# Optimization experiments

Measured on AMD Instinct MI355X. Metric: run time of the kernel, lower is better.

Reference implementation:

```python
import jax, jax.numpy as jnp
import numpy as np

UNITS = 1024
PRENET = 256
NMELS = 80
OPS = 2
ZONEOUT = 0.1  # deterministic (inference) zoneout blend


def _mi_lstm(x, wx, wh, alpha, b1, b2, bias):
    """Multiplicative-integration LSTM with deterministic zoneout.
    x: [B,T,D]; wx: [D,4U]; wh: [U,4U]; alpha/b1/b2/bias: [4U]."""
    B = x.shape[0]
    U = wh.shape[0]
    xw = jnp.einsum('btd,dk->btk', x, wx)  # precompute input projection [B,T,4U]

    def step(carry, xw_t):
        h, c = carry
        hw = h @ wh  # [B,4U]
        z = alpha * xw_t * hw + b1 * xw_t + b2 * hw + bias
        i, f, g, o = jnp.split(z, 4, axis=-1)
        c_new = jax.nn.sigmoid(f) * c + jax.nn.sigmoid(i) * jnp.tanh(g)
        h_new = jax.nn.sigmoid(o) * jnp.tanh(c_new)
        c_out = ZONEOUT * c + (1.0 - ZONEOUT) * c_new
        h_out = ZONEOUT * h + (1.0 - ZONEOUT) * h_new
        return (h_out, c_out), h_out

    init = (jnp.zeros((B, U), x.dtype), jnp.zeros((B, U), x.dtype))
    _, hs = jax.lax.scan(step, init, jnp.swapaxes(xw, 0, 1))  # [T,B,U]
    return jnp.swapaxes(hs, 0, 1)


def setup_inputs() -> dict:
    key = jax.random.key(0)
    ks = jax.random.split(key, 10)
    s = 0.02
    w = lambda k, shape: (jax.random.normal(k, shape, jnp.float32) * s)
    G = 4 * UNITS
    return {
        'x': jax.random.normal(ks[0], (32, 400, NMELS), jnp.float32),
        'pw1': w(ks[1], (NMELS, PRENET)), 'pb1': jnp.zeros((PRENET,), jnp.float32),
        'pw2': w(ks[2], (PRENET, PRENET)), 'pb2': jnp.zeros((PRENET,), jnp.float32),
        'wx1': w(ks[3], (PRENET, G)), 'wh1': w(ks[4], (UNITS, G)),
        'a1': jnp.ones((G,), jnp.float32), 'b11': jnp.full((G,), 0.5, jnp.float32),
        'b21': jnp.full((G,), 0.5, jnp.float32), 'bias1': jnp.zeros((G,), jnp.float32),
        'wx2': w(ks[5], (UNITS, G)), 'wh2': w(ks[6], (UNITS, G)),
        'a2': jnp.ones((G,), jnp.float32), 'b12': jnp.full((G,), 0.5, jnp.float32),
        'b22': jnp.full((G,), 0.5, jnp.float32), 'bias2': jnp.zeros((G,), jnp.float32),
        'sw': w(ks[7], (UNITS, 1)), 'sb': jnp.zeros((1,), jnp.float32),
        'fw': w(ks[8], (UNITS, NMELS * OPS)), 'fb': jnp.zeros((NMELS * OPS,), jnp.float32),
    }


def reference(x, pw1, pb1, pw2, pb2, wx1, wh1, a1, b11, b21, bias1,
              wx2, wh2, a2, b12, b22, bias2, sw, sb, fw, fb):
    # prenet (dropout inactive in inference-mode reference)
    p = jax.nn.relu(x @ pw1 + pb1)
    p = jax.nn.relu(p @ pw2 + pb2)
    h1 = _mi_lstm(p, wx1, wh1, a1, b11, b21, bias1)
    h2 = _mi_lstm(h1, wx2, wh2, a2, b12, b22, bias2)
    stop = jax.nn.sigmoid(h2 @ sw + sb)          # [B,T,1]
    frames = h2 @ fw + fb                         # [B,T,160] linear projection
    return jnp.concatenate([frames, stop], axis=-1)  # [B,T,161]
```

## Files before the change

### kernel.cpp

```cpp
#include <hip/hip_runtime.h>
#include <hip/hip_fp16.h>
#include <math.h>

#define B_   32
#define T_   400
#define BT_  12800
#define U_   1024
#define G4_  4096
#define TCH  100
#define NCH  4

typedef _Float16 f16x8 __attribute__((ext_vector_type(8)));
typedef float    f32x4 __attribute__((ext_vector_type(4)));

__device__ __forceinline__ float sigf(float x){ return 1.0f/(1.0f+expf(-x)); }
__device__ __forceinline__ int f2h2(float a, float b){
    __half2 h = __floats2half2_rn(a, b);
    return __builtin_bit_cast(int, h);
}
__device__ __forceinline__ f16x8 ldg8(const __half* p){
    return *reinterpret_cast<const f16x8*>(p);
}

__global__ __launch_bounds__(256) void ws_sentinel_kernel(float* __restrict__ out, int n)
{
    const int i = blockIdx.x * 256 + threadIdx.x;
    if (i < n) out[i] = 1000.0f;
}

__global__ __launch_bounds__(256) void transpose_fp16_kernel(
    const float* __restrict__ W, __half* __restrict__ WT, int rowsTotal)
{
    __shared__ float tile[64][65];
    const int bx = blockIdx.x;
    const int by = blockIdx.y;
    const int tid = threadIdx.x;
    for (int i = tid; i < 1024; i += 256) {
        const int r  = i >> 4;
        const int c4 = (i & 15) * 4;
        float4 v = *(const float4*)&W[(by*64 + r)*G4_ + bx*64 + c4];
        tile[c4+0][r] = v.x; tile[c4+1][r] = v.y;
        tile[c4+2][r] = v.z; tile[c4+3][r] = v.w;
    }
    __syncthreads();
    for (int i = tid; i < 512; i += 256) {
        const int c  = i >> 3;
        const int r8 = (i & 7) * 8;
        int4 pk;
        pk.x = f2h2(tile[c][r8+0], tile[c][r8+1]);
        pk.y = f2h2(tile[c][r8+2], tile[c][r8+3]);
        pk.z = f2h2(tile[c][r8+4], tile[c][r8+5]);
        pk.w = f2h2(tile[c][r8+6], tile[c][r8+7]);
        *(int4*)&WT[(size_t)(bx*64 + c)*rowsTotal + by*64 + r8] = pk;
    }
}

__global__ __launch_bounds__(256) void prenet_kernel(
    const float* __restrict__ x, const float* __restrict__ pw1, const float* __restrict__ pb1,
    const float* __restrict__ pw2, const float* __restrict__ pb2, __half* __restrict__ p)
{
    __shared__ float xs[32*80];
    __shared__ float ys[32*256];
    const int r0 = blockIdx.x * 32;
    const int tid = threadIdx.x;
    for (int i = tid; i < 32*80; i += 256) xs[i] = x[r0*80 + i];
    __syncthreads();
    const int j = tid;
    float acc[32];
    #pragma unroll
    for (int r=0;r<32;r++) acc[r] = pb1[j];
    for (int k=0;k<80;k++){
        float w = pw1[k*256 + j];
        #pragma unroll
        for (int r=0;r<32;r++) acc[r] += xs[r*80+k]*w;
    }
    #pragma unroll
    for (int r=0;r<32;r++) ys[r*256+j] = fmaxf(acc[r], 0.0f);
    __syncthreads();
    #pragma unroll
    for (int r=0;r<32;r++) acc[r] = pb2[j];
    for (int k=0;k<256;k++){
        float w = pw2[k*256 + j];
        #pragma unroll
        for (int r=0;r<32;r++) acc[r] += ys[r*256+k]*w;
    }
    #pragma unroll
    for (int r=0;r<32;r++) p[(r0+r)*256 + j] = __float2half_rn(fmaxf(acc[r], 0.0f));
}

__device__ __forceinline__ int groww(int l, int t0){
    const int bb = l / TCH;
    const int tt = l - bb*TCH;
    return bb*T_ + t0 + tt;
}

template<int K>
__global__ __launch_bounds__(256) void gemm_mfma(
    const __half* __restrict__ A, const __half* __restrict__ BT,
    __half* __restrict__ C, int t0)
{
    const int tid  = threadIdx.x;
    const int wid  = tid >> 6;
    const int lane = tid & 63;
    const int lr   = lane & 15;
    const int kg   = lane >> 4;
    const int wrow = wid >> 1;
    const int wcol = wid & 1;
    const int row0 = blockIdx.y*64 + wrow*32;
    const int col0 = blockIdx.x*64 + wcol*32;

    const int gr0 = groww(row0 + lr,      t0);
    const int gr1 = groww(row0 + 16 + lr, t0);
    const __half* a0p = &A[(size_t)gr0*K + kg*8];
    const __half* a1p = &A[(size_t)gr1*K + kg*8];
    const __half* b0p = &BT[(size_t)(col0 + lr)*K      + kg*8];
    const __half* b1p = &BT[(size_t)(col0 + 16 + lr)*K + kg*8];

    f32x4 acc00={0,0,0,0}, acc01={0,0,0,0}, acc10={0,0,0,0}, acc11={0,0,0,0};
    for (int k0 = 0; k0 < K; k0 += 32) {
        const f16x8 a0 = ldg8(a0p + k0);
        const f16x8 a1 = ldg8(a1p + k0);
        const f16x8 b0 = ldg8(b0p + k0);
        const f16x8 b1 = ldg8(b1p + k0);
        acc00 = __builtin_amdgcn_mfma_f32_16x16x32_f16(a0, b0, acc00, 0, 0, 0);
        acc01 = __builtin_amdgcn_mfma_f32_16x16x32_f16(a0, b1, acc01, 0, 0, 0);
        acc10 = __builtin_amdgcn_mfma_f32_16x16x32_f16(a1, b0, acc10, 0, 0, 0);
        acc11 = __builtin_amdgcn_mfma_f32_16x16x32_f16(a1, b1, acc11, 0, 0, 0);
    }
    #pragma unroll
    for (int r = 0; r < 4; r++) {
        const int rA = row0 + kg*4 + r, rB = row0 + 16 + kg*4 + r;
        const int cA = col0 + lr,       cB = col0 + 16 + lr;
        C[(size_t)rA*G4_ + cA] = __float2half_rn(acc00[r]);
        C[(size_t)rA*G4_ + cB] = __float2half_rn(acc01[r]);
        C[(size_t)rB*G4_ + cA] = __float2half_rn(acc10[r]);
        C[(size_t)rB*G4_ + cB] = __float2half_rn(acc11[r]);
    }
}

__global__ __launch_bounds__(256) void lstm_step(
    const __half* __restrict__ whT,
    const __half* __restrict__ xwc,
    const float* __restrict__ aP,  const float* __restrict__ b1P,
    const float* __restrict__ b2P, const float* __restrict__ biasP,
    const __half* __restrict__ hA,
    int rstride, int roff,
    const float* __restrict__ hprev,
    float* __restrict__ hout,
    float* __restrict__ c_st,
    __half* __restrict__ seq,
    int t, int tr)
{
    __shared__ float pt[4][32][17];
    const int tid  = threadIdx.x;
    const int wid  = tid >> 6;
    const int lane = tid & 63;
    const int lr   = lane & 15;
    const int kg   = lane >> 4;
    const int bu0  = blockIdx.x * 4;

    const __half* bp  = &whT[(size_t)((lr>>2)*U_ + bu0 + (lr&3))*U_ + wid*256 + kg*8];
    const __half* a0p = &hA[(size_t)(lr*rstride        + roff)*U_ + wid*256 + kg*8];
    const __half* a1p = &hA[(size_t)((lr+16)*rstride   + roff)*U_ + wid*256 + kg*8];

    f32x4 acc0={0,0,0,0}, acc1={0,0,0,0};
    #pragma unroll
    for (int ks = 0; ks < 8; ks++) {
        const f16x8 b  = ldg8(bp  + ks*32);
        const f16x8 a0 = ldg8(a0p + ks*32);
        const f16x8 a1 = ldg8(a1p + ks*32);
        acc0 = __builtin_amdgcn_mfma_f32_16x16x32_f16(a0, b, acc0, 0, 0, 0);
        acc1 = __builtin_amdgcn_mfma_f32_16x16x32_f16(a1, b, acc1, 0, 0, 0);
    }
    #pragma unroll
    for (int r = 0; r < 4; r++) {
        pt[wid][kg*4 + r][lr]      = acc0[r];
        pt[wid][16 + kg*4 + r][lr] = acc1[r];
    }
    __syncthreads();

    if (tid < 128) {
        const int bb = tid >> 2;
        const int j  = tid & 3;
        const int u  = bu0 + j;
        float hw[4];
        #pragma unroll
        for (int g = 0; g < 4; g++) {
            const int lc = g*4 + j;
            hw[g] = pt[0][bb][lc] + pt[1][bb][lc] + pt[2][bb][lc] + pt[3][bb][lc];
        }
        const __half* xwrow = &xwc[(size_t)(bb*TCH + tr) * G4_];
        const float x_i = __half2float(xwrow[0*U_ + u]);
        const float x_f = __half2float(xwrow[1*U_ + u]);
        const float x_g = __half2float(xwrow[2*U_ + u]);
        const float x_o = __half2float(xwrow[3*U_ + u]);
        const int ci = 0*U_+u, cf = 1*U_+u, cg = 2*U_+u, co = 3*U_+u;
        const float z_i = aP[ci]*x_i*hw[0] + b1P[ci]*x_i + b2P[ci]*hw[0] + biasP[ci];
        const float z_f = aP[cf]*x_f*hw[1] + b1P[cf]*x_f + b2P[cf]*hw[1] + biasP[cf];
        const float z_g = aP[cg]*x_g*hw[2] + b1P[cg]*x_g + b2P[cg]*hw[2] + biasP[cg];
        const float z_o = aP[co]*x_o*hw[3] + b1P[co]*x_o + b2P[co]*hw[3] + biasP[co];
        const float c_old  = c_st[bb*U_ + u];
        const float c_new  = sigf(z_f)*c_old + sigf(z_i)*tanhf(z_g);
        const float h_new  = sigf(z_o)*tanhf(c_new);
        const float c_outv = 0.1f*c_old + 0.9f*c_new;
        const float h_pv   = hprev[bb*U_ + u];
        const float h_outv = 0.1f*h_pv + 0.9f*h_new;
        c_st[bb*U_ + u]  = c_outv;
        hout[bb*U_ + u]  = h_outv;
        seq[(size_t)(bb*T_ + t)*U_ + u] = __float2half_rn(h_outv);
    }
}

__global__ __launch_bounds__(256) void final_kernel(
    const __half* __restrict__ h2, const float* __restrict__ fw, const float* __restrict__ fb,
    const float* __restrict__ sw, const float* __restrict__ sb, float* __restrict__ out)
{
    __shared__ float hs2[32*1028];
    const int r0 = blockIdx.x * 32;
    const int tid = threadIdx.x;
    for (int i = tid; i < 8192; i += 256) {
        const int r = i >> 8;
        const int k = (i & 255) * 4;
        const __half2* hp = (const __half2*)&h2[(size_t)(r0+r)*1024 + k];
        const float2 f0 = __half22float2(hp[0]);
        const float2 f1 = __half22float2(hp[1]);
        hs2[r*1028 + k+0] = f0.x; hs2[r*1028 + k+1] = f0.y;
        hs2[r*1028 + k+2] = f1.x; hs2[r*1028 + k+3] = f1.y;
    }
    __syncthreads();
    const int j = tid;
    if (j < 161) {
        const bool is_stop = (j == 160);
        float acc[32];
        const float bias = is_stop ? sb[0] : fb[j];
        #pragma unroll
        for (int r=0;r<32;r++) acc[r] = bias;
        for (int k=0;k<1024;k++){
            const float w = is_stop ? sw[k] : fw[k*160 + j];
            #pragma unroll
            for (int r=0;r<32;r++) acc[r] += hs2[r*1028 + k] * w;
        }
        #pragma unroll
        for (int r=0;r<32;r++){
            float v = acc[r];
            if (is_stop) v = sigf(v);
            out[(size_t)(r0+r)*161 + j] = v;
        }
    }
}

extern "C" void kernel_launch(void* const* d_in, const int* in_sizes, int n_in,
                              void* d_out, int out_size, void* d_ws, size_t ws_size,
                              hipStream_t stream)
{
    const float* x    = (const float*)d_in[0];
    const float* pw1  = (const float*)d_in[1];
    const float* pb1  = (const float*)d_in[2];
    const float* pw2  = (const float*)d_in[3];
    const float* pb2  = (const float*)d_in[4];
    const float* wx1  = (const float*)d_in[5];
    const float* wh1  = (const float*)d_in[6];
    const float* a1   = (const float*)d_in[7];
    const float* b11  = (const float*)d_in[8];
    const float* b21  = (const float*)d_in[9];
    const float* bias1= (const float*)d_in[10];
    const float* wx2  = (const float*)d_in[11];
    const float* wh2  = (const float*)d_in[12];
    const float* a2   = (const float*)d_in[13];
    const float* b12  = (const float*)d_in[14];
    const float* b22  = (const float*)d_in[15];
    const float* bias2= (const float*)d_in[16];
    const float* sw   = (const float*)d_in[17];
    const float* sb   = (const float*)d_in[18];
    const float* fw   = (const float*)d_in[19];
    const float* fb   = (const float*)d_in[20];
    float* out = (float*)d_out;

    char* base = (char*)d_ws;
    __half* hseq = (__half*)(base);
    __half* xwc  = (__half*)(base + 26214400);
    __half* p    = (__half*)(base + 52428800);
    float*  hb0  = (float*) (base + 58982400);
    float*  hb1  = (float*) (base + 59113472);
    float*  cb   = (float*) (base + 59244544);
    __half* whT1 = (__half*)(base + 59375616);
    __half* whT2 = (__half*)(base + 67764224);
    __half* wxT1 = (__half*)(base + 76152832);
    __half* wxT2 = (__half*)(base + 78249984);
    __half* h16z = (__half*)(base + 86638592);
    const size_t NEED = 86704128;
    if (ws_size < NEED) {
        ws_sentinel_kernel<<<(out_size + 255) / 256, 256, 0, stream>>>(out, out_size);
        return;
    }

    transpose_fp16_kernel<<<dim3(64,16), 256, 0, stream>>>(wh1, whT1, 1024);
    transpose_fp16_kernel<<<dim3(64,16), 256, 0, stream>>>(wh2, whT2, 1024);
    transpose_fp16_kernel<<<dim3(64, 4), 256, 0, stream>>>(wx1, wxT1, 256);
    transpose_fp16_kernel<<<dim3(64,16), 256, 0, stream>>>(wx2, wxT2, 1024);
    hipMemsetAsync(h16z, 0, 65536, stream);

    prenet_kernel<<<400, 256, 0, stream>>>(x, pw1, pb1, pw2, pb2, p);

    hipMemsetAsync(hb0, 0, (size_t)3*32768*sizeof(float), stream);
    for (int c = 0; c < NCH; c++) {
        const int t0 = c * TCH;
        gemm_mfma<256><<<dim3(64, 50), 256, 0, stream>>>(p, wxT1, xwc, t0);
        for (int tt = 0; tt < TCH; tt++) {
            const int t = t0 + tt;
            float* hin = (t & 1) ? hb1 : hb0;
            float* hou = (t & 1) ? hb0 : hb1;
            const __half* hA = (t == 0) ? h16z : hseq;
            const int rs = (t == 0) ? 1 : T_;
            const int ro = (t == 0) ? 0 : (t - 1);
            lstm_step<<<256, 256, 0, stream>>>(whT1, xwc, a1, b11, b21, bias1,
                                               hA, rs, ro, hin, hou, cb, hseq, t, tt);
        }
    }

    hipMemsetAsync(hb0, 0, (size_t)3*32768*sizeof(float), stream);
    for (int c = 0; c < NCH; c++) {
        const int t0 = c * TCH;
        gemm_mfma<1024><<<dim3(64, 50), 256, 0, stream>>>(hseq, wxT2, xwc, t0);
        for (int tt = 0; tt < TCH; tt++) {
            const int t = t0 + tt;
            float* hin = (t & 1) ? hb1 : hb0;
            float* hou = (t & 1) ? hb0 : hb1;
            const __half* hA = (t == 0) ? h16z : hseq;
            const int rs = (t == 0) ? 1 : T_;
            const int ro = (t == 0) ? 0 : (t - 1);
            lstm_step<<<256, 256, 0, stream>>>(whT2, xwc, a2, b12, b22, bias2,
                                               hA, rs, ro, hin, hou, cb, hseq, t, tt);
        }
    }

    final_kernel<<<400, 256, 0, stream>>>(hseq, fw, fb, sw, sb, out);
}
```

Baseline: 7.297 ms.

## Replace per-timestep LSTM launches with a persistent chunk kernel using a grid barrier

Each 100-step chunk of the recurrence now runs in one persistent kernel of 64 blocks, one per 16 hidden units across all four gates. Blocks synchronise between timesteps with a software grid barrier built on atomics instead of relaunching a kernel every step. This removes the launch overhead of hundreds of per-step kernels, and the per-unit gate parameters are cached in shared memory. The trade-offs are that only 64 CUs do the recurrent matmul, each wave runs a longer serial K loop, and progress depends on all 64 blocks being co-resident and on the barrier's cost.

```diff
diff --git a/kernel.cpp b/kernel.cpp
--- a/kernel.cpp
+++ b/kernel.cpp
@@ -138,76 +138,98 @@
     }
 }
 
-__global__ __launch_bounds__(256) void lstm_step(
+__device__ __forceinline__ void gridbar(int* cnt, int* gen, int nblk)
+{
+    __syncthreads();
+    if (threadIdx.x == 0) {
+        __threadfence();
+        const int g = atomicAdd(gen, 0);
+        if (atomicAdd(cnt, 1) == nblk - 1) {
+            atomicExch(cnt, 0);
+            __threadfence();
+            atomicAdd(gen, 1);
+        } else {
+            while (atomicAdd(gen, 0) == g) { __builtin_amdgcn_s_sleep(8); }
+        }
+        __threadfence();
+    }
+    __syncthreads();
+}
+
+__global__ __launch_bounds__(256) void lstm_chunk(
     const __half* __restrict__ whT,
     const __half* __restrict__ xwc,
     const float* __restrict__ aP,  const float* __restrict__ b1P,
     const float* __restrict__ b2P, const float* __restrict__ biasP,
-    const __half* __restrict__ hA,
-    int rstride, int roff,
-    const float* __restrict__ hprev,
-    float* __restrict__ hout,
+    float* __restrict__ hb0,
+    float* __restrict__ hb1,
     float* __restrict__ c_st,
     __half* __restrict__ seq,
-    int t, int tr)
+    int t0, int* bar_cnt, int* bar_gen)
 {
     __shared__ float pt[4][32][17];
+    __shared__ float prm[4][4][16];
     const int tid  = threadIdx.x;
     const int wid  = tid >> 6;
     const int lane = tid & 63;
     const int lr   = lane & 15;
     const int kg   = lane >> 4;
-    const int bu0  = blockIdx.x * 4;
-
-    const __half* bp  = &whT[(size_t)((lr>>2)*U_ + bu0 + (lr&3))*U_ + wid*256 + kg*8];
-    const __half* a0p = &hA[(size_t)(lr*rstride        + roff)*U_ + wid*256 + kg*8];
-    const __half* a1p = &hA[(size_t)((lr+16)*rstride   + roff)*U_ + wid*256 + kg*8];
-
-    f32x4 acc0={0,0,0,0}, acc1={0,0,0,0};
-    #pragma unroll
-    for (int ks = 0; ks < 8; ks++) {
-        const f16x8 b  = ldg8(bp  + ks*32);
-        const f16x8 a0 = ldg8(a0p + ks*32);
-        const f16x8 a1 = ldg8(a1p + ks*32);
-        acc0 = __builtin_amdgcn_mfma_f32_16x16x32_f16(a0, b, acc0, 0, 0, 0);
-        acc1 = __builtin_amdgcn_mfma_f32_16x16x32_f16(a1, b, acc1, 0, 0, 0);
-    }
-    #pragma unroll
-    for (int r = 0; r < 4; r++) {
-        pt[wid][kg*4 + r][lr]      = acc0[r];
-        pt[wid][16 + kg*4 + r][lr] = acc1[r];
-    }
-    __syncthreads();
-
-    if (tid < 128) {
-        const int bb = tid >> 2;
-        const int j  = tid & 3;
-        const int u  = bu0 + j;
-        float hw[4];
-        #pragma unroll
-        for (int g = 0; g < 4; g++) {
-            const int lc = g*4 + j;
-            hw[g] = pt[0][bb][lc] + pt[1][bb][lc] + pt[2][bb][lc] + pt[3][bb][lc];
-        }
-        const __half* xwrow = &xwc[(size_t)(bb*TCH + tr) * G4_];
-        const float x_i = __half2float(xwrow[0*U_ + u]);
-        const float x_f = __half2float(xwrow[1*U_ + u]);
-        const float x_g = __half2float(xwrow[2*U_ + u]);
-        const float x_o = __half2float(xwrow[3*U_ + u]);
-        const int ci = 0*U_+u, cf = 1*U_+u, cg = 2*U_+u, co = 3*U_+u;
-        const float z_i = aP[ci]*x_i*hw[0] + b1P[ci]*x_i + b2P[ci]*hw[0] + biasP[ci];
-        const float z_f = aP[cf]*x_f*hw[1] + b1P[cf]*x_f + b2P[cf]*hw[1] + biasP[cf];
-        const float z_g = aP[cg]*x_g*hw[2] + b1P[cg]*x_g + b2P[cg]*hw[2] + biasP[cg];
-        const float z_o = aP[co]*x_o*hw[3] + b1P[co]*x_o + b2P[co]*hw[3] + biasP[co];
-        const float c_old  = c_st[bb*U_ + u];
-        const float c_new  = sigf(z_f)*c_old + sigf(z_i)*tanhf(z_g);
-        const float h_new  = sigf(z_o)*tanhf(c_new);
-        const float c_outv = 0.1f*c_old + 0.9f*c_new;
-        const float h_pv   = hprev[bb*U_ + u];
-        const float h_outv = 0.1f*h_pv + 0.9f*h_new;
-        c_st[bb*U_ + u]  = c_outv;
-        hout[bb*U_ + u]  = h_outv;
-        seq[(size_t)(bb*T_ + t)*U_ + u] = __float2half_rn(h_outv);
+    const int u0   = blockIdx.x * 16;
+    const int nblk = gridDim.x;
+
+    if (tid < 64) {
+        const int g = tid >> 4, j = tid & 15, col = g*U_ + u0 + j;
+        prm[0][g][j] = aP[col];  prm[1][g][j] = b1P[col];
+        prm[2][g][j] = b2P[col]; prm[3][g][j] = biasP[col];
+    }
+    __syncthreads();
+
+    const __half* bp = &whT[(size_t)(wid*U_ + u0 + lr)*U_ + kg*8];
+
+    for (int tt = 0; tt < TCH; ++tt) {
+        const int t = t0 + tt;
+        f32x4 acc0 = {0,0,0,0}, acc1 = {0,0,0,0};
+        if (t > 0) {
+            const __half* a0p = &seq[(size_t)(lr*T_      + t-1)*U_ + kg*8];
+            const __half* a1p = &seq[(size_t)((lr+16)*T_ + t-1)*U_ + kg*8];
+            #pragma unroll 4
+            for (int ks = 0; ks < 32; ++ks) {
+                const f16x8 b  = ldg8(bp  + ks*32);
+                const f16x8 a0 = ldg8(a0p + ks*32);
+                const f16x8 a1 = ldg8(a1p + ks*32);
+                acc0 = __builtin_amdgcn_mfma_f32_16x16x32_f16(a0, b, acc0, 0, 0, 0);
+                acc1 = __builtin_amdgcn_mfma_f32_16x16x32_f16(a1, b, acc1, 0, 0, 0);
+            }
+        }
+        #pragma unroll
+        for (int r = 0; r < 4; r++) {
+            pt[wid][kg*4 + r][lr]      = acc0[r];
+            pt[wid][16 + kg*4 + r][lr] = acc1[r];
+        }
+        __syncthreads();
+
+        const float* hbR = (t & 1) ? hb0 : hb1;
+        float*       hbW = (t & 1) ? hb1 : hb0;
+        #pragma unroll
+        for (int o = tid; o < 512; o += 256) {
+            const int b = o >> 4, j = o & 15, u = u0 + j;
+            const __half* xr = &xwc[(size_t)(b*TCH + tt)*G4_];
+            float z[4];
+            #pragma unroll
+            for (int g = 0; g < 4; g++) {
+                const float hw = pt[g][b][j];
+                const float xw = __half2float(xr[g*U_ + u]);
+                z[g] = prm[0][g][j]*xw*hw + prm[1][g][j]*xw + prm[2][g][j]*hw + prm[3][g][j];
+            }
+            const float c_old = c_st[b*U_ + u];
+            const float c_new = sigf(z[1])*c_old + sigf(z[0])*tanhf(z[2]);
+            const float h_new = sigf(z[3])*tanhf(c_new);
+            c_st[b*U_ + u] = 0.1f*c_old + 0.9f*c_new;
+            const float h_out = 0.1f*hbR[b*U_ + u] + 0.9f*h_new;
+            hbW[b*U_ + u] = h_out;
+            seq[(size_t)(b*T_ + t)*U_ + u] = __float2half_rn(h_out);
+        }
+        gridbar(bar_cnt, bar_gen, nblk);
     }
 }
 
@@ -287,8 +309,8 @@
     __half* whT2 = (__half*)(base + 67764224);
     __half* wxT1 = (__half*)(base + 76152832);
     __half* wxT2 = (__half*)(base + 78249984);
-    __half* h16z = (__half*)(base + 86638592);
-    const size_t NEED = 86704128;
+    int*    bar  = (int*)   (base + 86638592);
+    const size_t NEED = 86638656;
     if (ws_size < NEED) {
         ws_sentinel_kernel<<<(out_size + 255) / 256, 256, 0, stream>>>(out, out_size);
         return;
@@ -298,7 +320,7 @@
     transpose_fp16_kernel<<<dim3(64,16), 256, 0, stream>>>(wh2, whT2, 1024);
     transpose_fp16_kernel<<<dim3(64, 4), 256, 0, stream>>>(wx1, wxT1, 256);
     transpose_fp16_kernel<<<dim3(64,16), 256, 0, stream>>>(wx2, wxT2, 1024);
-    hipMemsetAsync(h16z, 0, 65536, stream);
+    hipMemsetAsync(bar, 0, 64, stream);
 
     prenet_kernel<<<400, 256, 0, stream>>>(x, pw1, pb1, pw2, pb2, p);
 
@@ -306,32 +328,16 @@
     for (int c = 0; c < NCH; c++) {
         const int t0 = c * TCH;
         gemm_mfma<256><<<dim3(64, 50), 256, 0, stream>>>(p, wxT1, xwc, t0);
-        for (int tt = 0; tt < TCH; tt++) {
-            const int t = t0 + tt;
-            float* hin = (t & 1) ? hb1 : hb0;
-            float* hou = (t & 1) ? hb0 : hb1;
-            const __half* hA = (t == 0) ? h16z : hseq;
-            const int rs = (t == 0) ? 1 : T_;
-            const int ro = (t == 0) ? 0 : (t - 1);
-            lstm_step<<<256, 256, 0, stream>>>(whT1, xwc, a1, b11, b21, bias1,
-                                               hA, rs, ro, hin, hou, cb, hseq, t, tt);
-        }
+        lstm_chunk<<<64, 256, 0, stream>>>(whT1, xwc, a1, b11, b21, bias1,
+                                           hb0, hb1, cb, hseq, t0, bar, bar+1);
     }
 
     hipMemsetAsync(hb0, 0, (size_t)3*32768*sizeof(float), stream);
     for (int c = 0; c < NCH; c++) {
         const int t0 = c * TCH;
         gemm_mfma<1024><<<dim3(64, 50), 256, 0, stream>>>(hseq, wxT2, xwc, t0);
-        for (int tt = 0; tt < TCH; tt++) {
-            const int t = t0 + tt;
-            float* hin = (t & 1) ? hb1 : hb0;
-            float* hou = (t & 1) ? hb0 : hb1;
-            const __half* hA = (t == 0) ? h16z : hseq;
-            const int rs = (t == 0) ? 1 : T_;
-            const int ro = (t == 0) ? 0 : (t - 1);
-            lstm_step<<<256, 256, 0, stream>>>(whT2, xwc, a2, b12, b22, bias2,
-                                               hA, rs, ro, hin, hou, cb, hseq, t, tt);
-        }
+        lstm_chunk<<<64, 256, 0, stream>>>(whT2, xwc, a2, b12, b22, bias2,
+                                           hb0, hb1, cb, hseq, t0, bar, bar+1);
     }
 
     final_kernel<<<400, 256, 0, stream>>>(hseq, fw, fb, sw, sb, out);
```

After: 17.22 ms. +136.0%, slower.

## Wavefront-fuse both LSTM layers into one per-step kernel with inline input projection

Applied to the files above, without the earlier changes.

Replaces the chunked input-projection GEMMs and the 800 per-layer step launches with 401 launches of a single kernel. Each launch runs layer 1 at step t and layer 2 at step t-1 in separate blocks, and computes the input projection for that step inside the kernel. This halves the number of launches, lets the two layers overlap, and removes the xw scratch buffer and the fp32 h buffers, since the previous h is now read back from the fp16 sequence. The cost is that the input projection runs as many small per-step GEMMs instead of large batched ones. The layer-2 blocks also do a K=1024 input GEMM on every step, which lengthens the critical path, and the zoneout blend now uses an h rounded to fp16.

```diff
diff --git a/kernel.cpp b/kernel.cpp
--- a/kernel.cpp
+++ b/kernel.cpp
@@ -7,8 +7,6 @@
 #define BT_  12800
 #define U_   1024
 #define G4_  4096
-#define TCH  100
-#define NCH  4
 
 typedef _Float16 f16x8 __attribute__((ext_vector_type(8)));
 typedef float    f32x4 __attribute__((ext_vector_type(4)));
@@ -88,126 +86,102 @@
     for (int r=0;r<32;r++) p[(r0+r)*256 + j] = __float2half_rn(fmaxf(acc[r], 0.0f));
 }
 
-__device__ __forceinline__ int groww(int l, int t0){
-    const int bb = l / TCH;
-    const int tt = l - bb*TCH;
-    return bb*T_ + t0 + tt;
-}
-
-template<int K>
-__global__ __launch_bounds__(256) void gemm_mfma(
-    const __half* __restrict__ A, const __half* __restrict__ BT,
-    __half* __restrict__ C, int t0)
-{
+__global__ __launch_bounds__(256) void fused_step(
+    const __half* __restrict__ whT1, const __half* __restrict__ wxT1,
+    const __half* __restrict__ whT2, const __half* __restrict__ wxT2,
+    const __half* __restrict__ p,
+    __half* __restrict__ h1seq, __half* __restrict__ h2seq,
+    const float* __restrict__ a1, const float* __restrict__ b11,
+    const float* __restrict__ b21, const float* __restrict__ bias1,
+    const float* __restrict__ a2, const float* __restrict__ b12,
+    const float* __restrict__ b22, const float* __restrict__ bias2,
+    float* __restrict__ c1, float* __restrict__ c2, int t)
+{
+    const bool isL2 = blockIdx.x >= 256;
+    const int s = isL2 ? (t - 1) : t;
+    if (s < 0 || s >= T_) return;
+
+    const __half* whT = isL2 ? whT2 : whT1;
+    const __half* wiT = isL2 ? wxT2 : wxT1;
+    const __half* xin = isL2 ? h1seq : p;
+    const int     KX  = isL2 ? 1024 : 256;
+    const __half* hrc = isL2 ? h2seq : h1seq;
+    __half*      seqW = isL2 ? h2seq : h1seq;
+    const float* aP   = isL2 ? a2 : a1;
+    const float* b1P  = isL2 ? b12 : b11;
+    const float* b2P  = isL2 ? b22 : b21;
+    const float* bsP  = isL2 ? bias2 : bias1;
+    float*       cst  = isL2 ? c2 : c1;
+
+    __shared__ float pt[4][32][17];
+    __shared__ float px[4][32][17];
     const int tid  = threadIdx.x;
     const int wid  = tid >> 6;
     const int lane = tid & 63;
     const int lr   = lane & 15;
     const int kg   = lane >> 4;
-    const int wrow = wid >> 1;
-    const int wcol = wid & 1;
-    const int row0 = blockIdx.y*64 + wrow*32;
-    const int col0 = blockIdx.x*64 + wcol*32;
-
-    const int gr0 = groww(row0 + lr,      t0);
-    const int gr1 = groww(row0 + 16 + lr, t0);
-    const __half* a0p = &A[(size_t)gr0*K + kg*8];
-    const __half* a1p = &A[(size_t)gr1*K + kg*8];
-    const __half* b0p = &BT[(size_t)(col0 + lr)*K      + kg*8];
-    const __half* b1p = &BT[(size_t)(col0 + 16 + lr)*K + kg*8];
-
-    f32x4 acc00={0,0,0,0}, acc01={0,0,0,0}, acc10={0,0,0,0}, acc11={0,0,0,0};
-    for (int k0 = 0; k0 < K; k0 += 32) {
-        const f16x8 a0 = ldg8(a0p + k0);
-        const f16x8 a1 = ldg8(a1p + k0);
-        const f16x8 b0 = ldg8(b0p + k0);
-        const f16x8 b1 = ldg8(b1p + k0);
-        acc00 = __builtin_amdgcn_mfma_f32_16x16x32_f16(a0, b0, acc00, 0, 0, 0);
-        acc01 = __builtin_amdgcn_mfma_f32_16x16x32_f16(a0, b1, acc01, 0, 0, 0);
-        acc10 = __builtin_amdgcn_mfma_f32_16x16x32_f16(a1, b0, acc10, 0, 0, 0);
-        acc11 = __builtin_amdgcn_mfma_f32_16x16x32_f16(a1, b1, acc11, 0, 0, 0);
+    const int u0   = (blockIdx.x & 255) * 4;
+    const int lcrow = (lr >> 2)*U_ + u0 + (lr & 3);
+
+    f32x4 aH0 = {0,0,0,0}, aH1 = {0,0,0,0};
+    if (s > 0) {
+        const __half* bp  = &whT[(size_t)lcrow*U_ + wid*256 + kg*8];
+        const __half* a0p = &hrc[(size_t)(lr*T_      + s-1)*U_ + wid*256 + kg*8];
+        const __half* a1p = &hrc[(size_t)((lr+16)*T_ + s-1)*U_ + wid*256 + kg*8];
+        #pragma unroll
+        for (int ks = 0; ks < 8; ks++) {
+            const f16x8 b  = ldg8(bp  + ks*32);
+            const f16x8 x0 = ldg8(a0p + ks*32);
+            const f16x8 x1 = ldg8(a1p + ks*32);
+            aH0 = __builtin_amdgcn_mfma_f32_16x16x32_f16(x0, b, aH0, 0, 0, 0);
+            aH1 = __builtin_amdgcn_mfma_f32_16x16x32_f16(x1, b, aH1, 0, 0, 0);
+        }
+    }
+    f32x4 aX0 = {0,0,0,0}, aX1 = {0,0,0,0};
+    {
+        const int kw = KX >> 2;
+        const __half* bp  = &wiT[(size_t)lcrow*KX + wid*kw + kg*8];
+        const __half* a0p = &xin[(size_t)(lr*T_      + s)*KX + wid*kw + kg*8];
+        const __half* a1p = &xin[(size_t)((lr+16)*T_ + s)*KX + wid*kw + kg*8];
+        const int it = kw >> 5;
+        for (int ks = 0; ks < it; ks++) {
+            const f16x8 b  = ldg8(bp  + ks*32);
+            const f16x8 x0 = ldg8(a0p + ks*32);
+            const f16x8 x1 = ldg8(a1p + ks*32);
+            aX0 = __builtin_amdgcn_mfma_f32_16x16x32_f16(x0, b, aX0, 0, 0, 0);
+            aX1 = __builtin_amdgcn_mfma_f32_16x16x32_f16(x1, b, aX1, 0, 0, 0);
+        }
     }
     #pragma unroll
     for (int r = 0; r < 4; r++) {
-        const int rA = row0 + kg*4 + r, rB = row0 + 16 + kg*4 + r;
-        const int cA = col0 + lr,       cB = col0 + 16 + lr;
-        C[(size_t)rA*G4_ + cA] = __float2half_rn(acc00[r]);
-        C[(size_t)rA*G4_ + cB] = __float2half_rn(acc01[r]);
-        C[(size_t)rB*G4_ + cA] = __float2half_rn(acc10[r]);
-        C[(size_t)rB*G4_ + cB] = __float2half_rn(acc11[r]);
-    }
-}
-
-__global__ __launch_bounds__(256) void lstm_step(
-    const __half* __restrict__ whT,
-    const __half* __restrict__ xwc,
-    const float* __restrict__ aP,  const float* __restrict__ b1P,
-    const float* __restrict__ b2P, const float* __restrict__ biasP,
-    const __half* __restrict__ hA,
-    int rstride, int roff,
-    const float* __restrict__ hprev,
-    float* __restrict__ hout,
-    float* __restrict__ c_st,
-    __half* __restrict__ seq,
-    int t, int tr)
-{
-    __shared__ float pt[4][32][17];
-    const int tid  = threadIdx.x;
-    const int wid  = tid >> 6;
-    const int lane = tid & 63;
-    const int lr   = lane & 15;
-    const int kg   = lane >> 4;
-    const int bu0  = blockIdx.x * 4;
-
-    const __half* bp  = &whT[(size_t)((lr>>2)*U_ + bu0 + (lr&3))*U_ + wid*256 + kg*8];
-    const __half* a0p = &hA[(size_t)(lr*rstride        + roff)*U_ + wid*256 + kg*8];
-    const __half* a1p = &hA[(size_t)((lr+16)*rstride   + roff)*U_ + wid*256 + kg*8];
-
-    f32x4 acc0={0,0,0,0}, acc1={0,0,0,0};
-    #pragma unroll
-    for (int ks = 0; ks < 8; ks++) {
-        const f16x8 b  = ldg8(bp  + ks*32);
-        const f16x8 a0 = ldg8(a0p + ks*32);
-        const f16x8 a1 = ldg8(a1p + ks*32);
-        acc0 = __builtin_amdgcn_mfma_f32_16x16x32_f16(a0, b, acc0, 0, 0, 0);
-        acc1 = __builtin_amdgcn_mfma_f32_16x16x32_f16(a1, b, acc1, 0, 0, 0);
-    }
-    #pragma unroll
-    for (int r = 0; r < 4; r++) {
-        pt[wid][kg*4 + r][lr]      = acc0[r];
-        pt[wid][16 + kg*4 + r][lr] = acc1[r];
+        pt[wid][kg*4 + r][lr]      = aH0[r];
+        pt[wid][16 + kg*4 + r][lr] = aH1[r];
+        px[wid][kg*4 + r][lr]      = aX0[r];
+        px[wid][16 + kg*4 + r][lr] = aX1[r];
     }
     __syncthreads();
 
     if (tid < 128) {
         const int bb = tid >> 2;
         const int j  = tid & 3;
-        const int u  = bu0 + j;
-        float hw[4];
+        const int u  = u0 + j;
+        float z[4];
         #pragma unroll
         for (int g = 0; g < 4; g++) {
             const int lc = g*4 + j;
-            hw[g] = pt[0][bb][lc] + pt[1][bb][lc] + pt[2][bb][lc] + pt[3][bb][lc];
-        }
-        const __half* xwrow = &xwc[(size_t)(bb*TCH + tr) * G4_];
-        const float x_i = __half2float(xwrow[0*U_ + u]);
-        const float x_f = __half2float(xwrow[1*U_ + u]);
-        const float x_g = __half2float(xwrow[2*U_ + u]);
-        const float x_o = __half2float(xwrow[3*U_ + u]);
-        const int ci = 0*U_+u, cf = 1*U_+u, cg = 2*U_+u, co = 3*U_+u;
-        const float z_i = aP[ci]*x_i*hw[0] + b1P[ci]*x_i + b2P[ci]*hw[0] + biasP[ci];
-        const float z_f = aP[cf]*x_f*hw[1] + b1P[cf]*x_f + b2P[cf]*hw[1] + biasP[cf];
-        const float z_g = aP[cg]*x_g*hw[2] + b1P[cg]*x_g + b2P[cg]*hw[2] + biasP[cg];
-        const float z_o = aP[co]*x_o*hw[3] + b1P[co]*x_o + b2P[co]*hw[3] + biasP[co];
-        const float c_old  = c_st[bb*U_ + u];
-        const float c_new  = sigf(z_f)*c_old + sigf(z_i)*tanhf(z_g);
-        const float h_new  = sigf(z_o)*tanhf(c_new);
-        const float c_outv = 0.1f*c_old + 0.9f*c_new;
-        const float h_pv   = hprev[bb*U_ + u];
-        const float h_outv = 0.1f*h_pv + 0.9f*h_new;
-        c_st[bb*U_ + u]  = c_outv;
-        hout[bb*U_ + u]  = h_outv;
-        seq[(size_t)(bb*T_ + t)*U_ + u] = __float2half_rn(h_outv);
+            const float hw = pt[0][bb][lc] + pt[1][bb][lc] + pt[2][bb][lc] + pt[3][bb][lc];
+            const float xw = px[0][bb][lc] + px[1][bb][lc] + px[2][bb][lc] + px[3][bb][lc];
+            const int col = g*U_ + u;
+            z[g] = aP[col]*xw*hw + b1P[col]*xw + b2P[col]*hw + bsP[col];
+        }
+        const float c_old = (s > 0) ? cst[bb*U_ + u] : 0.0f;
+        const float c_new = sigf(z[1])*c_old + sigf(z[0])*tanhf(z[2]);
+        const float h_new = sigf(z[3])*tanhf(c_new);
+        cst[bb*U_ + u] = 0.1f*c_old + 0.9f*c_new;
+        const float h_prev = (s > 0)
+            ? __half2float(seqW[(size_t)(bb*T_ + s-1)*U_ + u]) : 0.0f;
+        const float h_out = 0.1f*h_prev + 0.9f*h_new;
+        seqW[(size_t)(bb*T_ + s)*U_ + u] = __float2half_rn(h_out);
     }
 }
 
@@ -277,18 +251,16 @@
     float* out = (float*)d_out;
 
     char* base = (char*)d_ws;
-    __half* hseq = (__half*)(base);
-    __half* xwc  = (__half*)(base + 26214400);
-    __half* p    = (__half*)(base + 52428800);
-    float*  hb0  = (float*) (base + 58982400);
-    float*  hb1  = (float*) (base + 59113472);
-    float*  cb   = (float*) (base + 59244544);
-    __half* whT1 = (__half*)(base + 59375616);
-    __half* whT2 = (__half*)(base + 67764224);
-    __half* wxT1 = (__half*)(base + 76152832);
-    __half* wxT2 = (__half*)(base + 78249984);
-    __half* h16z = (__half*)(base + 86638592);
-    const size_t NEED = 86704128;
+    __half* h1seq = (__half*)(base);
+    __half* h2seq = (__half*)(base + 26214400);
+    __half* p     = (__half*)(base + 52428800);
+    __half* whT1  = (__half*)(base + 58982400);
+    __half* whT2  = (__half*)(base + 67371008);
+    __half* wxT1  = (__half*)(base + 75759616);
+    __half* wxT2  = (__half*)(base + 77856768);
+    float*  c1    = (float*) (base + 86245376);
+    float*  c2    = (float*) (base + 86376448);
+    const size_t NEED = 86507520;
     if (ws_size < NEED) {
         ws_sentinel_kernel<<<(out_size + 255) / 256, 256, 0, stream>>>(out, out_size);
         return;
@@ -298,41 +270,16 @@
     transpose_fp16_kernel<<<dim3(64,16), 256, 0, stream>>>(wh2, whT2, 1024);
     transpose_fp16_kernel<<<dim3(64, 4), 256, 0, stream>>>(wx1, wxT1, 256);
     transpose_fp16_kernel<<<dim3(64,16), 256, 0, stream>>>(wx2, wxT2, 1024);
-    hipMemsetAsync(h16z, 0, 65536, stream);
 
     prenet_kernel<<<400, 256, 0, stream>>>(x, pw1, pb1, pw2, pb2, p);
 
-    hipMemsetAsync(hb0, 0, (size_t)3*32768*sizeof(float), stream);
-    for (int c = 0; c < NCH; c++) {
-        const int t0 = c * TCH;
-        gemm_mfma<256><<<dim3(64, 50), 256, 0, stream>>>(p, wxT1, xwc, t0);
-        for (int tt = 0; tt < TCH; tt++) {
-            const int t = t0 + tt;
-            float* hin = (t & 1) ? hb1 : hb0;
-            float* hou = (t & 1) ? hb0 : hb1;
-            const __half* hA = (t == 0) ? h16z : hseq;
-            const int rs = (t == 0) ? 1 : T_;
-            const int ro = (t == 0) ? 0 : (t - 1);
-            lstm_step<<<256, 256, 0, stream>>>(whT1, xwc, a1, b11, b21, bias1,
-                                               hA, rs, ro, hin, hou, cb, hseq, t, tt);
-        }
-    }
-
-    hipMemsetAsync(hb0, 0, (size_t)3*32768*sizeof(float), stream);
-    for (int c = 0; c < NCH; c++) {
-        const int t0 = c * TCH;
-        gemm_mfma<1024><<<dim3(64, 50), 256, 0, stream>>>(hseq, wxT2, xwc, t0);
-        for (int tt = 0; tt < TCH; tt++) {
-            const int t = t0 + tt;
-            float* hin = (t & 1) ? hb1 : hb0;
-            float* hou = (t & 1) ? hb0 : hb1;
-            const __half* hA = (t == 0) ? h16z : hseq;
-            const int rs = (t == 0) ? 1 : T_;
-            const int ro = (t == 0) ? 0 : (t - 1);
-            lstm_step<<<256, 256, 0, stream>>>(whT2, xwc, a2, b12, b22, bias2,
-                                               hA, rs, ro, hin, hou, cb, hseq, t, tt);
-        }
-    }
-
-    final_kernel<<<400, 256, 0, stream>>>(hseq, fw, fb, sw, sb, out);
-}
+    for (int t = 0; t <= T_; t++) {
+        fused_step<<<512, 256, 0, stream>>>(whT1, wxT1, whT2, wxT2, p,
+                                            h1seq, h2seq,
+                                            a1, b11, b21, bias1,
+                                            a2, b12, b22, bias2,
+                                            c1, c2, t);
+    }
+
+    final_kernel<<<400, 256, 0, stream>>>(h2seq, fw, fb, sw, sb, out);
+}
```

Result: faster. 6.070 ms (-16.8%).
